# Performance work log

Hardware: AMD Instinct MI355X
Metric: run time of the kernel (lower is better)

The kernel has to match this reference:

```python
import jax, jax.numpy as jnp
import numpy as np

D_MODEL = 1024
HEAD_SIZE = 64
B, T = 4, 4096


def setup_inputs() -> dict:
    key = jax.random.key(0)
    k1, k2, k3, k4, k5, k6 = jax.random.split(key, 6)
    q = jax.random.normal(k1, (B, T, D_MODEL), dtype=jnp.float32)
    k = jax.random.normal(k2, (B, T, D_MODEL), dtype=jnp.float32)
    v = jax.random.normal(k3, (B, T, D_MODEL), dtype=jnp.float32)
    # bias-free Linear weights stored as [d_model, head_size] so proj = x @ W
    s = 1.0 / np.sqrt(D_MODEL)
    Wq = jax.random.uniform(k4, (D_MODEL, HEAD_SIZE), jnp.float32, -s, s)
    Wk = jax.random.uniform(k5, (D_MODEL, HEAD_SIZE), jnp.float32, -s, s)
    Wv = jax.random.uniform(k6, (D_MODEL, HEAD_SIZE), jnp.float32, -s, s)
    # [T,T] bool mask, True = keep (lower-triangular, exercises masking path)
    attn_mask = jnp.tril(jnp.ones((T, T), dtype=jnp.bool_))
    return {"q": q, "k": k, "v": v, "Wq": Wq, "Wk": Wk, "Wv": Wv,
            "attn_mask": attn_mask}


def reference(q, k, v, Wq, Wk, Wv, attn_mask):
    # projections: [B,T,d_model] @ [d_model,head] -> [B,T,head]
    qh = q @ Wq
    kh = k @ Wk
    vh = v @ Wv
    # raw scores [B,T,T]; attention_operation is Identity
    att = jnp.einsum('bqh,bkh->bqk', qh, kh)
    # mask BEFORE scaling (matches original; -inf/scale == -inf)
    att = jnp.where(attn_mask[None, :, :], att, -jnp.inf)
    scale = jnp.asarray(HEAD_SIZE ** 0.5, att.dtype)
    probs = jax.nn.softmax(att / scale, axis=-1)
    # dropout rate is 0.0 -> no-op
    return jnp.einsum('bqk,bkh->bqh', probs, vh)
```

## Files before the change

kernel.cpp:

```cpp
#include <hip/hip_runtime.h>
#include <hip/hip_fp16.h>

typedef _Float16 f16;
typedef __fp16 h16x2 __attribute__((ext_vector_type(2)));
typedef _Float16 f16x8 __attribute__((ext_vector_type(8)));
typedef _Float16 f16x4v __attribute__((ext_vector_type(4)));
typedef float f32x4 __attribute__((ext_vector_type(4)));
typedef float f32x16 __attribute__((ext_vector_type(16)));
typedef unsigned int u32;
typedef u32 u32x4 __attribute__((ext_vector_type(4)));

constexpr int DM = 1024;
constexpr int HS = 64;
constexpr int NBATCH = 4;
constexpr int T = 4096;
constexpr float CEXP = 0.18033688011112042f;

#if __has_builtin(__builtin_amdgcn_exp2f)
#define EXP2(x) __builtin_amdgcn_exp2f(x)
#else
#define EXP2(x) exp2f(x)
#endif

static __device__ __forceinline__ u32 pack2_f16(float a, float b) {
  union { f16 h[2]; u32 u; } cv;
  cv.h[0] = (f16)a; cv.h[1] = (f16)b;
  return cv.u;
}

static __device__ __forceinline__ f16x8 cvt8(const f32x4& a0, const f32x4& a1) {
  union { h16x2 p[4]; f16x8 v; } cv;
  cv.p[0] = __builtin_amdgcn_cvt_pkrtz(a0[0], a0[1]);
  cv.p[1] = __builtin_amdgcn_cvt_pkrtz(a0[2], a0[3]);
  cv.p[2] = __builtin_amdgcn_cvt_pkrtz(a1[0], a1[1]);
  cv.p[3] = __builtin_amdgcn_cvt_pkrtz(a1[2], a1[3]);
  return cv.v;
}

__global__ void wtrans_kernel(const float* __restrict__ Wq, const float* __restrict__ Wk,
                              const float* __restrict__ Wv, f16* __restrict__ WTf) {
  const int which = blockIdx.y;
  const float* __restrict__ W = (which == 0) ? Wq : ((which == 1) ? Wk : Wv);
  const int o8 = blockIdx.x * 256 + threadIdx.x;
  const int t = o8 >> 8;
  const int cb = (o8 >> 6) & 3;
  const int g = (o8 >> 4) & 3;
  const int q15 = o8 & 15;
  const int col = cb * 16 + q15;
  f16x8 v;
#pragma unroll
  for (int e = 0; e < 8; ++e) v[e] = (f16)W[(t * 32 + 8 * g + e) * 64 + col];
  *(f16x8*)(WTf + which * 65536 + o8 * 8) = v;
}

__global__ __launch_bounds__(256, 6) void proj_kernel(
    const float* __restrict__ xq, const float* __restrict__ xk, const float* __restrict__ xv,
    const f16* __restrict__ WTf, f16* __restrict__ qh, f16* __restrict__ kh,
    f16* __restrict__ vhT) {
  __shared__ float sR[4][64][17];

  const int which = blockIdx.y;
  const float* __restrict__ x = (which == 0) ? xq : ((which == 1) ? xk : xv);
  const int tid = threadIdx.x;
  const int lane = tid & 63, w = tid >> 6;
  const int q15 = lane & 15, g = lane >> 4;
  const int tile = w >> 1, khalf = w & 1;
  const int rowblk = blockIdx.x * 32;
  const int row0t = rowblk + tile * 16;

  const float* __restrict__ xrow = x + (size_t)(row0t + q15) * DM + khalf * 512 + 8 * g;
  const char* __restrict__ wfb =
      (const char*)(WTf + which * 65536) + (size_t)khalf * 65536 + lane * 16;

  f32x4 acc[4];
#pragma unroll
  for (int cb = 0; cb < 4; ++cb) acc[cb] = (f32x4){0.f, 0.f, 0.f, 0.f};

#pragma unroll 2
  for (int t = 0; t < 16; ++t) {
    const f32x4 a0 = *(const f32x4*)(xrow + t * 32);
    const f32x4 a1 = *(const f32x4*)(xrow + t * 32 + 4);
    const f16x8 af = cvt8(a0, a1);
    const char* wfrag = wfb + (size_t)t * 4096;
    const f16x8 b0 = *(const f16x8*)(wfrag);
    const f16x8 b1 = *(const f16x8*)(wfrag + 1024);
    const f16x8 b2 = *(const f16x8*)(wfrag + 2048);
    const f16x8 b3 = *(const f16x8*)(wfrag + 3072);
    acc[0] = __builtin_amdgcn_mfma_f32_16x16x32_f16(af, b0, acc[0], 0, 0, 0);
    acc[1] = __builtin_amdgcn_mfma_f32_16x16x32_f16(af, b1, acc[1], 0, 0, 0);
    acc[2] = __builtin_amdgcn_mfma_f32_16x16x32_f16(af, b2, acc[2], 0, 0, 0);
    acc[3] = __builtin_amdgcn_mfma_f32_16x16x32_f16(af, b3, acc[3], 0, 0, 0);
  }

#pragma unroll
  for (int cb = 0; cb < 4; ++cb)
#pragma unroll
    for (int j = 0; j < 4; ++j) sR[w][lane][cb * 4 + j] = acc[cb][j];
  __syncthreads();

  const int tile2 = tid >> 7;
  const int t7 = tid & 127;
  const int c15 = t7 & 15;
  const int g2 = (t7 >> 4) & 3;
  const int cbb = (t7 >> 6) * 2;
  const int srcLane = g2 * 16 + c15;
  const int orow0 = rowblk + tile2 * 16;

#pragma unroll
  for (int ci = 0; ci < 2; ++ci) {
    const int cb = cbb + ci;
    float vals[4];
#pragma unroll
    for (int j = 0; j < 4; ++j)
      vals[j] = sR[tile2 * 2][srcLane][cb * 4 + j] + sR[tile2 * 2 + 1][srcLane][cb * 4 + j];
    if (which < 2) {
      f16* __restrict__ outp = (which == 0) ? qh : kh;
#pragma unroll
      for (int j = 0; j < 4; ++j)
        outp[(size_t)(orow0 + 4 * g2 + j) * HS + cb * 16 + c15] = (f16)vals[j];
    } else {
      const int b = orow0 >> 12;
      const int t0 = (orow0 & (T - 1)) + 4 * g2;
      f16x4v pv;
#pragma unroll
      for (int j = 0; j < 4; ++j) pv[j] = (f16)vals[j];
      *(f16x4v*)(vhT + (size_t)b * HS * T + (size_t)(cb * 16 + c15) * T + t0) = pv;
    }
  }
}

__global__ __launch_bounds__(512, 4) void attn_kernel(
    const f16* __restrict__ qh, const f16* __restrict__ kh,
    const f16* __restrict__ vhT, float* __restrict__ out) {
  __shared__ float sO[4][64][33];
  __shared__ float sMm[8][32];
  __shared__ float sLs[8][32];

  const int tid = threadIdx.x;
  const int lane = tid & 63, w = tid >> 6;
  const int q31 = lane & 31, hi = lane >> 5;

  const int id = blockIdx.x;
  const int b = (id & 7) >> 1;
  const int qt = 127 - 2 * (id >> 3) - (id & 1);
  const int q0 = qt * 32;

  const f16* __restrict__ kbase = kh + (size_t)b * T * HS;
  const f16* __restrict__ vbase = vhT + (size_t)b * HS * T;
  const f16* __restrict__ qp = qh + (size_t)(b * T + q0 + q31) * HS + 8 * hi;

  f16x8 qb[4];
#pragma unroll
  for (int kt = 0; kt < 4; ++kt) qb[kt] = *(const f16x8*)(qp + 16 * kt);

  f32x16 o0, o1;
#pragma unroll
  for (int i = 0; i < 16; ++i) { o0[i] = 0.f; o1[i] = 0.f; }
  float m = -1e30f, lsum = 0.f;

  const int nblk = qt + 1;
  for (int blk = w; blk < nblk; blk += 8) {
    const int kv0 = blk * 32;
    const f16* kr = kbase + (size_t)(kv0 + q31) * HS + 8 * hi;
    f16x8 ka0 = *(const f16x8*)(kr);
    f16x8 ka1 = *(const f16x8*)(kr + 16);
    f16x8 ka2 = *(const f16x8*)(kr + 32);
    f16x8 ka3 = *(const f16x8*)(kr + 48);

    f32x16 s;
#pragma unroll
    for (int i = 0; i < 16; ++i) s[i] = 0.f;
    s = __builtin_amdgcn_mfma_f32_32x32x16_f16(ka0, qb[0], s, 0, 0, 0);
    s = __builtin_amdgcn_mfma_f32_32x32x16_f16(ka1, qb[1], s, 0, 0, 0);
    s = __builtin_amdgcn_mfma_f32_32x32x16_f16(ka2, qb[2], s, 0, 0, 0);
    s = __builtin_amdgcn_mfma_f32_32x32x16_f16(ka3, qb[3], s, 0, 0, 0);

    const f16* vr = vbase + (size_t)q31 * T + kv0 + 8 * hi;
    f16x8 v00 = *(const f16x8*)(vr);
    f16x8 v01 = *(const f16x8*)(vr + 16);
    f16x8 v10 = *(const f16x8*)(vr + (size_t)32 * T);
    f16x8 v11 = *(const f16x8*)(vr + (size_t)32 * T + 16);

    if (blk == qt) {
#pragma unroll
      for (int r = 0; r < 16; ++r) {
        const int kl = (r & 3) + 8 * (r >> 2) + 4 * hi;
        if (kl > q31) s[r] = -1e30f;
      }
    }

    float pm = s[0];
#pragma unroll
    for (int r = 1; r < 16; ++r) pm = fmaxf(pm, s[r]);
    pm = fmaxf(pm, __shfl_xor(pm, 32));
    if (!__all(pm <= m + 32.f)) {
      const float mn = fmaxf(m, pm);
      const float r = EXP2((m - mn) * CEXP);
      lsum *= r;
#pragma unroll
      for (int i = 0; i < 16; ++i) { o0[i] *= r; o1[i] *= r; }
      m = mn;
    }

    float p[16];
    float ps = 0.f;
#pragma unroll
    for (int r = 0; r < 16; ++r) { p[r] = EXP2((s[r] - m) * CEXP); ps += p[r]; }
    ps += __shfl_xor(ps, 32);
    lsum += ps;

    u32 c[8], x[8];
#pragma unroll
    for (int i = 0; i < 8; ++i) c[i] = pack2_f16(p[2 * i], p[2 * i + 1]);
#pragma unroll
    for (int i = 0; i < 8; ++i) x[i] = (u32)__shfl_xor((int)c[i], 32);
    union { u32x4 u; f16x8 f; } f1, f2;
    f1.u = (u32x4){ hi ? x[2] : c[0], hi ? x[3] : c[1], hi ? c[2] : x[0], hi ? c[3] : x[1] };
    f2.u = (u32x4){ hi ? x[6] : c[4], hi ? x[7] : c[5], hi ? c[6] : x[4], hi ? c[7] : x[5] };

    o0 = __builtin_amdgcn_mfma_f32_32x32x16_f16(v00, f1.f, o0, 0, 0, 0);
    o0 = __builtin_amdgcn_mfma_f32_32x32x16_f16(v01, f2.f, o0, 0, 0, 0);
    o1 = __builtin_amdgcn_mfma_f32_32x32x16_f16(v10, f1.f, o1, 0, 0, 0);
    o1 = __builtin_amdgcn_mfma_f32_32x32x16_f16(v11, f2.f, o1, 0, 0, 0);
  }

  if (lane < 32) sMm[w][q31] = m;
  __syncthreads();
  float M = sMm[0][q31];
#pragma unroll
  for (int w2 = 1; w2 < 8; ++w2) M = fmaxf(M, sMm[w2][q31]);
  const float sc = EXP2((m - M) * CEXP);
  if (lane < 32) sLs[w][q31] = lsum * sc;
#pragma unroll
  for (int i = 0; i < 16; ++i) { o0[i] *= sc; o1[i] *= sc; }

  if (w >= 4) {
#pragma unroll
    for (int r = 0; r < 16; ++r) {
      const int d = (r & 3) + 8 * (r >> 2) + 4 * hi;
      sO[w - 4][d][q31] = o0[r];
      sO[w - 4][d + 32][q31] = o1[r];
    }
  }
  __syncthreads();
  if (w < 4) {
#pragma unroll
    for (int r = 0; r < 16; ++r) {
      const int d = (r & 3) + 8 * (r >> 2) + 4 * hi;
      sO[w][d][q31] += o0[r];
      sO[w][d + 32][q31] += o1[r];
    }
  }
  __syncthreads();

  const int q = tid >> 4;
  const int d0 = (tid & 15) * 4;
  float L = 0.f;
#pragma unroll
  for (int w2 = 0; w2 < 8; ++w2) L += sLs[w2][q];
  const float invL = 1.f / L;
  float4 rv;
  rv.x = (sO[0][d0 + 0][q] + sO[1][d0 + 0][q] + sO[2][d0 + 0][q] + sO[3][d0 + 0][q]) * invL;
  rv.y = (sO[0][d0 + 1][q] + sO[1][d0 + 1][q] + sO[2][d0 + 1][q] + sO[3][d0 + 1][q]) * invL;
  rv.z = (sO[0][d0 + 2][q] + sO[1][d0 + 2][q] + sO[2][d0 + 2][q] + sO[3][d0 + 2][q]) * invL;
  rv.w = (sO[0][d0 + 3][q] + sO[1][d0 + 3][q] + sO[2][d0 + 3][q] + sO[3][d0 + 3][q]) * invL;
  *(float4*)(out + (size_t)(b * T + q0 + q) * HS + d0) = rv;
}

extern "C" void kernel_launch(void* const* d_in, const int* in_sizes, int n_in,
                              void* d_out, int out_size, void* d_ws, size_t ws_size,
                              hipStream_t stream) {
  const float* q  = (const float*)d_in[0];
  const float* k  = (const float*)d_in[1];
  const float* v  = (const float*)d_in[2];
  const float* Wq = (const float*)d_in[3];
  const float* Wk = (const float*)d_in[4];
  const float* Wv = (const float*)d_in[5];
  float* out = (float*)d_out;

  f16* qh  = (f16*)d_ws;
  f16* kh  = qh  + (size_t)NBATCH * T * HS;
  f16* vhT = kh  + (size_t)NBATCH * T * HS;
  f16* WTf = vhT + (size_t)NBATCH * T * HS;

  wtrans_kernel<<<dim3(32, 3), 256, 0, stream>>>(Wq, Wk, Wv, WTf);
  proj_kernel<<<dim3(512, 3), 256, 0, stream>>>(q, k, v, WTf, qh, kh, vhT);
  attn_kernel<<<dim3(T / 32 * NBATCH), 512, 0, stream>>>(qh, kh, vhT, out);
}
```

Before: 93.07 us.

## Restructure projection kernel with async global-to-LDS loads and 8-way K split

The projection kernel now gives each 512-thread block 16 rows, and each of its 8 waves owns a 128-wide K slice. Activations are staged into LDS through direct global_load_lds with an XOR swizzle, and each wave keeps its weight fragments in registers. Partial sums from all 8 waves are reduced through LDS, and the vhT write becomes a packed pair of halves. The aim is more memory-level parallelism for the large fp32 activation read, at the cost of more blocks, more register pressure and an 8-way LDS reduction.

Measured after the change: 96.75 us. 4.0% more time.

```diff
diff --git a/kernel.cpp b/kernel.cpp
--- a/kernel.cpp
+++ b/kernel.cpp
@@ -35,6 +35,12 @@
   cv.p[2] = __builtin_amdgcn_cvt_pkrtz(a1[0], a1[1]);
   cv.p[3] = __builtin_amdgcn_cvt_pkrtz(a1[2], a1[3]);
   return cv.v;
+}
+
+static __device__ __forceinline__ void gload_lds16(const void* g, void* l) {
+  __builtin_amdgcn_global_load_lds(
+      (__attribute__((address_space(1))) void*)(g),
+      (__attribute__((address_space(3))) void*)(l), 16, 0, 0);
 }
 
 __global__ void wtrans_kernel(const float* __restrict__ Wq, const float* __restrict__ Wk,
@@ -53,79 +59,82 @@
   *(f16x8*)(WTf + which * 65536 + o8 * 8) = v;
 }
 
-__global__ __launch_bounds__(256, 6) void proj_kernel(
+__global__ __launch_bounds__(512, 4) void proj_kernel(
     const float* __restrict__ xq, const float* __restrict__ xk, const float* __restrict__ xv,
     const f16* __restrict__ WTf, f16* __restrict__ qh, f16* __restrict__ kh,
     f16* __restrict__ vhT) {
-  __shared__ float sR[4][64][17];
+  __shared__ __align__(16) char As[8][8192];
 
   const int which = blockIdx.y;
   const float* __restrict__ x = (which == 0) ? xq : ((which == 1) ? xk : xv);
   const int tid = threadIdx.x;
   const int lane = tid & 63, w = tid >> 6;
   const int q15 = lane & 15, g = lane >> 4;
-  const int tile = w >> 1, khalf = w & 1;
-  const int rowblk = blockIdx.x * 32;
-  const int row0t = rowblk + tile * 16;
-
-  const float* __restrict__ xrow = x + (size_t)(row0t + q15) * DM + khalf * 512 + 8 * g;
-  const char* __restrict__ wfb =
-      (const char*)(WTf + which * 65536) + (size_t)khalf * 65536 + lane * 16;
+  const int row0 = blockIdx.x * 16;
+  const char* __restrict__ xbase = (const char*)x;
+
+  const int l7 = lane & 7, l3 = lane >> 3;
+  const int swz = ((l7 ^ l3) * 16);
+#pragma unroll
+  for (int t = 0; t < 4; ++t)
+#pragma unroll
+    for (int j = 0; j < 2; ++j) {
+      const int r = 8 * j + l3;
+      gload_lds16(xbase + (size_t)(row0 + r) * 4096 + (size_t)(w * 128 + t * 32) * 4 + swz,
+                  &As[w][t * 2048 + j * 1024]);
+    }
+
+  const char* __restrict__ wfb = (const char*)(WTf + which * 65536) + lane * 16;
+  f16x8 B[16];
+#pragma unroll
+  for (int i = 0; i < 16; ++i)
+    B[i] = *(const f16x8*)(wfb + (size_t)(w * 16 + i) * 1024);
+
+  asm volatile("s_waitcnt vmcnt(0)" ::: "memory");
+  __builtin_amdgcn_sched_barrier(0);
 
   f32x4 acc[4];
 #pragma unroll
   for (int cb = 0; cb < 4; ++cb) acc[cb] = (f32x4){0.f, 0.f, 0.f, 0.f};
 
-#pragma unroll 2
-  for (int t = 0; t < 16; ++t) {
-    const f32x4 a0 = *(const f32x4*)(xrow + t * 32);
-    const f32x4 a1 = *(const f32x4*)(xrow + t * 32 + 4);
+  const char* pa = &As[w][0] + q15 * 128;
+  const int rx = (q15 & 7) * 16;
+#pragma unroll
+  for (int t = 0; t < 4; ++t) {
+    const f32x4 a0 = *(const f32x4*)(pa + t * 2048 + (((2 * g + 0) * 16) ^ rx));
+    const f32x4 a1 = *(const f32x4*)(pa + t * 2048 + (((2 * g + 1) * 16) ^ rx));
     const f16x8 af = cvt8(a0, a1);
-    const char* wfrag = wfb + (size_t)t * 4096;
-    const f16x8 b0 = *(const f16x8*)(wfrag);
-    const f16x8 b1 = *(const f16x8*)(wfrag + 1024);
-    const f16x8 b2 = *(const f16x8*)(wfrag + 2048);
-    const f16x8 b3 = *(const f16x8*)(wfrag + 3072);
-    acc[0] = __builtin_amdgcn_mfma_f32_16x16x32_f16(af, b0, acc[0], 0, 0, 0);
-    acc[1] = __builtin_amdgcn_mfma_f32_16x16x32_f16(af, b1, acc[1], 0, 0, 0);
-    acc[2] = __builtin_amdgcn_mfma_f32_16x16x32_f16(af, b2, acc[2], 0, 0, 0);
-    acc[3] = __builtin_amdgcn_mfma_f32_16x16x32_f16(af, b3, acc[3], 0, 0, 0);
-  }
-
+#pragma unroll
+    for (int cb = 0; cb < 4; ++cb)
+      acc[cb] = __builtin_amdgcn_mfma_f32_16x16x32_f16(af, B[t * 4 + cb], acc[cb], 0, 0, 0);
+  }
+
+  float* part = (float*)&As[w][0];
 #pragma unroll
   for (int cb = 0; cb < 4; ++cb)
 #pragma unroll
-    for (int j = 0; j < 4; ++j) sR[w][lane][cb * 4 + j] = acc[cb][j];
-  __syncthreads();
-
-  const int tile2 = tid >> 7;
-  const int t7 = tid & 127;
-  const int c15 = t7 & 15;
-  const int g2 = (t7 >> 4) & 3;
-  const int cbb = (t7 >> 6) * 2;
-  const int srcLane = g2 * 16 + c15;
-  const int orow0 = rowblk + tile2 * 16;
-
-#pragma unroll
-  for (int ci = 0; ci < 2; ++ci) {
-    const int cb = cbb + ci;
-    float vals[4];
-#pragma unroll
     for (int j = 0; j < 4; ++j)
-      vals[j] = sR[tile2 * 2][srcLane][cb * 4 + j] + sR[tile2 * 2 + 1][srcLane][cb * 4 + j];
-    if (which < 2) {
-      f16* __restrict__ outp = (which == 0) ? qh : kh;
-#pragma unroll
-      for (int j = 0; j < 4; ++j)
-        outp[(size_t)(orow0 + 4 * g2 + j) * HS + cb * 16 + c15] = (f16)vals[j];
-    } else {
-      const int b = orow0 >> 12;
-      const int t0 = (orow0 & (T - 1)) + 4 * g2;
-      f16x4v pv;
-#pragma unroll
-      for (int j = 0; j < 4; ++j) pv[j] = (f16)vals[j];
-      *(f16x4v*)(vhT + (size_t)b * HS * T + (size_t)(cb * 16 + c15) * T + t0) = pv;
-    }
+      part[(4 * g + j) * 68 + cb * 16 + q15] = acc[cb][j];
+  __syncthreads();
+
+  const int col = tid & 63;
+  const int rp = (tid >> 6) * 2;
+  float v0 = 0.f, v1 = 0.f;
+#pragma unroll
+  for (int w2 = 0; w2 < 8; ++w2) {
+    const float* p2 = (const float*)&As[w2][0];
+    v0 += p2[rp * 68 + col];
+    v1 += p2[(rp + 1) * 68 + col];
+  }
+
+  if (which < 2) {
+    f16* __restrict__ outp = (which == 0) ? qh : kh;
+    outp[(size_t)(row0 + rp) * HS + col] = (f16)v0;
+    outp[(size_t)(row0 + rp + 1) * HS + col] = (f16)v1;
+  } else {
+    const int b = row0 >> 12;
+    const int trow = (row0 & (T - 1)) + rp;
+    *(u32*)(vhT + (size_t)b * HS * T + (size_t)col * T + trow) = pack2_f16(v0, v1);
   }
 }
 
@@ -209,14 +218,14 @@
     ps += __shfl_xor(ps, 32);
     lsum += ps;
 
-    u32 c[8], x[8];
+    u32 c[8], xg[8];
 #pragma unroll
     for (int i = 0; i < 8; ++i) c[i] = pack2_f16(p[2 * i], p[2 * i + 1]);
 #pragma unroll
-    for (int i = 0; i < 8; ++i) x[i] = (u32)__shfl_xor((int)c[i], 32);
+    for (int i = 0; i < 8; ++i) xg[i] = (u32)__shfl_xor((int)c[i], 32);
     union { u32x4 u; f16x8 f; } f1, f2;
-    f1.u = (u32x4){ hi ? x[2] : c[0], hi ? x[3] : c[1], hi ? c[2] : x[0], hi ? c[3] : x[1] };
-    f2.u = (u32x4){ hi ? x[6] : c[4], hi ? x[7] : c[5], hi ? c[6] : x[4], hi ? c[7] : x[5] };
+    f1.u = (u32x4){ hi ? xg[2] : c[0], hi ? xg[3] : c[1], hi ? c[2] : xg[0], hi ? c[3] : xg[1] };
+    f2.u = (u32x4){ hi ? xg[6] : c[4], hi ? xg[7] : c[5], hi ? c[6] : xg[4], hi ? c[7] : xg[5] };
 
     o0 = __builtin_amdgcn_mfma_f32_32x32x16_f16(v00, f1.f, o0, 0, 0, 0);
     o0 = __builtin_amdgcn_mfma_f32_32x32x16_f16(v01, f2.f, o0, 0, 0, 0);
@@ -284,6 +293,6 @@
   f16* WTf = vhT + (size_t)NBATCH * T * HS;
 
   wtrans_kernel<<<dim3(32, 3), 256, 0, stream>>>(Wq, Wk, Wv, WTf);
-  proj_kernel<<<dim3(512, 3), 256, 0, stream>>>(q, k, v, WTf, qh, kh, vhT);
+  proj_kernel<<<dim3(NBATCH * T / 16, 3), 512, 0, stream>>>(q, k, v, WTf, qh, kh, vhT);
   attn_kernel<<<dim3(T / 32 * NBATCH), 512, 0, stream>>>(qh, kh, vhT, out);
 }
```
